# Optimization experiments

Measured on AMD Instinct MI355X. Metric: run time of the kernel, lower is better.

The kernel has to match this reference:

```python
import jax, jax.numpy as jnp
import numpy as np

D_MODEL = 1024
H = 16
D_K = D_MODEL // H
B, S = 4, 2048
NEG = -1000000000.0


def setup_inputs() -> dict:
    key = jax.random.key(0)
    ks = jax.random.split(key, 12)
    scale = 1.0 / np.sqrt(D_MODEL)
    inp = {
        "query": jax.random.normal(ks[0], (B, S, D_MODEL), jnp.float32),
        "key": jax.random.normal(ks[1], (B, S, D_MODEL), jnp.float32),
        "value": jax.random.normal(ks[2], (B, S, D_MODEL), jnp.float32),
        # causal lower-triangular mask, shape (B, S, S); forward unsqueezes head dim
        "mask": jnp.broadcast_to(jnp.tril(jnp.ones((S, S), jnp.int32)), (B, S, S)),
        "Wq": jax.random.normal(ks[3], (D_MODEL, D_MODEL), jnp.float32) * scale,
        "bq": jnp.zeros((D_MODEL,), jnp.float32),
        "Wk": jax.random.normal(ks[4], (D_MODEL, D_MODEL), jnp.float32) * scale,
        "bk": jnp.zeros((D_MODEL,), jnp.float32),
        "Wv": jax.random.normal(ks[5], (D_MODEL, D_MODEL), jnp.float32) * scale,
        "bv": jnp.zeros((D_MODEL,), jnp.float32),
        "Wo": jax.random.normal(ks[6], (D_MODEL, D_MODEL), jnp.float32) * scale,
        "bo": jnp.zeros((D_MODEL,), jnp.float32),
    }
    return inp


def reference(query, key, value, mask, Wq, bq, Wk, bk, Wv, bv, Wo, bo):
    b, s, _ = query.shape
    # projections (torch Linear: x @ W.T + b); split into heads -> (b, h, s, d_k)
    def proj(x, W, bias):
        return (x @ W.T + bias).reshape(b, -1, H, D_K).transpose(0, 2, 1, 3)

    Q = proj(query, Wq, bq)
    K = proj(key, Wk, bk)
    V = proj(value, Wv, bv)

    scores = jnp.einsum("bhqd,bhkd->bhqk", Q, K) / np.sqrt(D_K)
    m = mask[:, None, :, :]  # (b, 1, s, s)
    scores = jnp.where(m == 0, NEG, scores)
    attn = jax.nn.softmax(scores, axis=-1)
    x = jnp.einsum("bhqk,bhkd->bhqd", attn, V)
    x = x.transpose(0, 2, 1, 3).reshape(b, -1, D_MODEL)
    return x @ Wo.T + bo
```

## Files before the change

kernel.cpp:

```cpp
#include <hip/hip_runtime.h>
#include <hip/hip_bf16.h>

#define DMODEL 1024
#define NH 16
#define DKH 64
#define NB 4
#define SEQ 2048
#define MTOT (NB*SEQ)

typedef __bf16 bf16_t;
typedef __bf16 bf16x8 __attribute__((ext_vector_type(8)));
typedef float f32x4 __attribute__((ext_vector_type(4)));

__device__ __forceinline__ void async_copy16(void* lds, const void* g) {
    __builtin_amdgcn_global_load_lds(
        (const __attribute__((address_space(1))) unsigned int*)g,
        (__attribute__((address_space(3))) unsigned int*)lds, 16, 0, 0);
}

__device__ __forceinline__ float fast_exp2(float x) {
    return __builtin_amdgcn_exp2f(x);
}

__device__ __forceinline__ float rsum16(float v) {
    v += __shfl_xor(v, 1);
    v += __shfl_xor(v, 2);
    v += __shfl_xor(v, 4);
    v += __shfl_xor(v, 8);
    return v;
}

__global__ void cvt_kernel(const float* __restrict__ s0, const float* __restrict__ s1,
                           const float* __restrict__ s2, const float* __restrict__ s3,
                           bf16_t* __restrict__ d0, bf16_t* __restrict__ d1,
                           bf16_t* __restrict__ d2, bf16_t* __restrict__ d3, int n)
{
    const float* s = (blockIdx.y == 0) ? s0 : (blockIdx.y == 1) ? s1 :
                     (blockIdx.y == 2) ? s2 : s3;
    bf16_t* d = (blockIdx.y == 0) ? d0 : (blockIdx.y == 1) ? d1 :
                (blockIdx.y == 2) ? d2 : d3;
    int i = (blockIdx.x * 256 + threadIdx.x) * 8;
    if (i < n) {
        float4 a = *(const float4*)&s[i];
        float4 b = *(const float4*)&s[i + 4];
        union { bf16_t h[8]; uint4 u; } t;
        t.h[0]=(bf16_t)a.x; t.h[1]=(bf16_t)a.y; t.h[2]=(bf16_t)a.z; t.h[3]=(bf16_t)a.w;
        t.h[4]=(bf16_t)b.x; t.h[5]=(bf16_t)b.y; t.h[6]=(bf16_t)b.z; t.h[7]=(bf16_t)b.w;
        *(uint4*)&d[i] = t.u;
    }
}

template<int OUT_MODE>
__global__ __launch_bounds__(256, 3)
void gemm_bt(const bf16_t* __restrict__ A, const bf16_t* __restrict__ W,
             const float* __restrict__ bias, void* __restrict__ out,
             int M, int N, int K, float scale)
{
    __shared__ bf16_t As[128 * 64];
    __shared__ bf16_t Ws[128 * 64];

    const int tid  = threadIdx.x;
    const int wave = tid >> 6;
    const int lane = tid & 63;
    const int ln   = lane & 15;
    const int quad = lane >> 4;
    const int wm   = (wave >> 1) * 64;
    const int wn   = (wave & 1) * 64;
    const int bm   = blockIdx.x * 128;
    const int bn   = blockIdx.y * 128;
    const int srow = wave * 8 + (lane >> 3);
    const int sg   = (lane & 7) * 8;

    f32x4 acc[4][4] = {};

    for (int k0 = 0; k0 < K; k0 += 64) {
        #pragma unroll
        for (int rr = 0; rr < 4; ++rr) {
            int row = rr * 32 + srow;
            async_copy16(&As[(size_t)(rr * 32 + wave * 8) * 64],
                         &A[(size_t)(bm + row) * K + k0 + sg]);
            async_copy16(&Ws[(size_t)(rr * 32 + wave * 8) * 64],
                         &W[(size_t)(bn + row) * K + k0 + sg]);
        }
        __syncthreads();

        bf16x8 af[2][4], wf[2][4];
        #pragma unroll
        for (int h = 0; h < 2; ++h)
            #pragma unroll
            for (int u = 0; u < 4; ++u) {
                af[h][u] = *(const bf16x8*)&As[(wm + u * 16 + ln) * 64 + h * 32 + quad * 8];
                wf[h][u] = *(const bf16x8*)&Ws[(wn + u * 16 + ln) * 64 + h * 32 + quad * 8];
            }
        #pragma unroll
        for (int h = 0; h < 2; ++h)
            #pragma unroll
            for (int im = 0; im < 4; ++im)
                #pragma unroll
                for (int jn = 0; jn < 4; ++jn)
                    acc[im][jn] = __builtin_amdgcn_mfma_f32_16x16x32_bf16(
                        af[h][im], wf[h][jn], acc[im][jn], 0, 0, 0);

        __syncthreads();
    }

    #pragma unroll
    for (int jn = 0; jn < 4; ++jn) {
        int n = bn + wn + jn * 16 + ln;
        float bv = bias[n];
        #pragma unroll
        for (int im = 0; im < 4; ++im) {
            #pragma unroll
            for (int r = 0; r < 4; ++r) {
                int m = bm + wm + im * 16 + quad * 4 + r;
                float v = (acc[im][jn][r] + bv) * scale;
                if (OUT_MODE == 0) {
                    int b = m >> 11, s = m & (SEQ - 1);
                    int h = n >> 6, d = n & 63;
                    ((bf16_t*)out)[(((size_t)(b * NH + h)) * SEQ + s) * DKH + d] = (bf16_t)v;
                } else if (OUT_MODE == 2) {
                    int b = m >> 11, s = m & (SEQ - 1);
                    int h = n >> 6, d = n & 63;
                    ((bf16_t*)out)[(((size_t)(b * NH + h)) * DKH + d) * SEQ + s] = (bf16_t)v;
                } else {
                    ((float*)out)[(size_t)m * N + n] = v;
                }
            }
        }
    }
}

__global__ __launch_bounds__(256, 3)
void gemm_qkv(const bf16_t* __restrict__ Aq, const bf16_t* __restrict__ Ak,
              const bf16_t* __restrict__ Av, const bf16_t* __restrict__ W3,
              const float* __restrict__ bqp, const float* __restrict__ bkp,
              const float* __restrict__ bvp,
              bf16_t* __restrict__ Qh, bf16_t* __restrict__ Kh,
              bf16_t* __restrict__ Vth, float qscale)
{
    __shared__ bf16_t As[128 * 64];
    __shared__ bf16_t Ws[128 * 64];

    const int K    = DMODEL;
    const int tid  = threadIdx.x;
    const int wave = tid >> 6;
    const int lane = tid & 63;
    const int ln   = lane & 15;
    const int quad = lane >> 4;
    const int wm   = (wave >> 1) * 64;
    const int wn   = (wave & 1) * 64;
    const int bm   = blockIdx.x * 128;
    const int bnG  = blockIdx.y * 128;
    const int sel  = blockIdx.y >> 3;
    const bf16_t* A = (sel == 0) ? Aq : (sel == 1) ? Ak : Av;
    const int srow = wave * 8 + (lane >> 3);
    const int sg   = (lane & 7) * 8;

    f32x4 acc[4][4] = {};

    for (int k0 = 0; k0 < K; k0 += 64) {
        #pragma unroll
        for (int rr = 0; rr < 4; ++rr) {
            int row = rr * 32 + srow;
            async_copy16(&As[(size_t)(rr * 32 + wave * 8) * 64],
                         &A[(size_t)(bm + row) * K + k0 + sg]);
            async_copy16(&Ws[(size_t)(rr * 32 + wave * 8) * 64],
                         &W3[(size_t)(bnG + row) * K + k0 + sg]);
        }
        __syncthreads();

        bf16x8 af[2][4], wf[2][4];
        #pragma unroll
        for (int h = 0; h < 2; ++h)
            #pragma unroll
            for (int u = 0; u < 4; ++u) {
                af[h][u] = *(const bf16x8*)&As[(wm + u * 16 + ln) * 64 + h * 32 + quad * 8];
                wf[h][u] = *(const bf16x8*)&Ws[(wn + u * 16 + ln) * 64 + h * 32 + quad * 8];
            }
        #pragma unroll
        for (int h = 0; h < 2; ++h)
            #pragma unroll
            for (int im = 0; im < 4; ++im)
                #pragma unroll
                for (int jn = 0; jn < 4; ++jn)
                    acc[im][jn] = __builtin_amdgcn_mfma_f32_16x16x32_bf16(
                        af[h][im], wf[h][jn], acc[im][jn], 0, 0, 0);

        __syncthreads();
    }

    const float* bias = (sel == 0) ? bqp : (sel == 1) ? bkp : bvp;
    const float scale = (sel == 0) ? qscale : 1.0f;
    const int bn = bnG & (DMODEL - 1);

    #pragma unroll
    for (int jn = 0; jn < 4; ++jn) {
        int n = bn + wn + jn * 16 + ln;
        float bv = bias[n];
        int h = n >> 6, d = n & 63;
        #pragma unroll
        for (int im = 0; im < 4; ++im) {
            #pragma unroll
            for (int r = 0; r < 4; ++r) {
                int m = bm + wm + im * 16 + quad * 4 + r;
                float v = (acc[im][jn][r] + bv) * scale;
                int b = m >> 11, s = m & (SEQ - 1);
                if (sel == 2) {
                    Vth[(((size_t)(b * NH + h)) * DKH + d) * SEQ + s] = (bf16_t)v;
                } else {
                    bf16_t* outp = (sel == 1) ? Kh : Qh;
                    outp[(((size_t)(b * NH + h)) * SEQ + s) * DKH + d] = (bf16_t)v;
                }
            }
        }
    }
}

__global__ __launch_bounds__(256, 3)
void attn_kernel(const bf16_t* __restrict__ Q, const bf16_t* __restrict__ Km,
                 const bf16_t* __restrict__ Vt, bf16_t* __restrict__ X)
{
    __shared__ __align__(16) bf16_t Ks[2][64 * 64];
    __shared__ __align__(16) bf16_t Vs[2][64 * 64];
    __shared__ __align__(16) bf16_t Ps[4][32][72];

    const int tid  = threadIdx.x;
    const int wave = tid >> 6;
    const int lane = tid & 63;
    const int ln   = lane & 15;
    const int quad = lane >> 4;
    const int cs   = ln & 7;

    const int qt = (blockIdx.x + blockIdx.y + ((blockIdx.y >> 4) << 2)) & 15;
    const int bh = blockIdx.y;
    const int q0 = qt * 128;
    const size_t base = (size_t)bh * SEQ * DKH;

    bf16x8 aq[2][2];
    #pragma unroll
    for (int so = 0; so < 2; ++so) {
        const bf16_t* qr = Q + base + (size_t)(q0 + so * 64 + wave * 16 + ln) * DKH;
        aq[so][0] = *(const bf16x8*)(qr + quad * 8);
        aq[so][1] = *(const bf16x8*)(qr + 32 + quad * 8);
    }

    f32x4 oacc[2][4] = {};
    float psum[2][4] = {};

    const int nkt = 2 * qt + 2;

    const int srow8 = lane >> 3;
    const int schk  = lane & 7;

    #pragma unroll
    for (int qq = 0; qq < 2; ++qq) {
        const int rb  = wave * 16 + qq * 8;
        const int row = rb + srow8;
        const int csr = schk ^ (row & 7);
        async_copy16(&Ks[0][rb * 64], Km + base + (size_t)row * DKH + csr * 8);
        async_copy16(&Vs[0][rb * 64], Vt + base + (size_t)row * SEQ + csr * 8);
    }
    __syncthreads();

    int cur = 0;
    for (int kt = 0; kt < nkt; ++kt, cur ^= 1) {
        const int j0 = kt * 64;
        const bool skip0 = (kt == nkt - 1);

        if (kt + 1 < nkt) {
            const int jn0 = j0 + 64;
            #pragma unroll
            for (int qq = 0; qq < 2; ++qq) {
                const int rb  = wave * 16 + qq * 8;
                const int row = rb + srow8;
                const int csr = schk ^ (row & 7);
                async_copy16(&Ks[cur ^ 1][rb * 64],
                             Km + base + (size_t)(jn0 + row) * DKH + csr * 8);
                async_copy16(&Vs[cur ^ 1][rb * 64],
                             Vt + base + (size_t)row * SEQ + jn0 + csr * 8);
            }
        }

        bf16x8 kf[4][2];
        #pragma unroll
        for (int jn = 0; jn < 4; ++jn) {
            const int rr = (jn * 16 + ln) * 64;
            kf[jn][0] = *(const bf16x8*)&Ks[cur][rr + ((quad    ) ^ cs) * 8];
            kf[jn][1] = *(const bf16x8*)&Ks[cur][rr + ((4 + quad) ^ cs) * 8];
        }

        f32x4 s[2][4] = {};
        #pragma unroll
        for (int so = 0; so < 2; ++so) {
            if (so == 0 && skip0) continue;
            #pragma unroll
            for (int jn = 0; jn < 4; ++jn) {
                s[so][jn] = __builtin_amdgcn_mfma_f32_16x16x32_bf16(aq[so][0], kf[jn][0], s[so][jn], 0, 0, 0);
                s[so][jn] = __builtin_amdgcn_mfma_f32_16x16x32_bf16(aq[so][1], kf[jn][1], s[so][jn], 0, 0, 0);
            }
        }

        bf16x8 vf[4][2];
        #pragma unroll
        for (int nj = 0; nj < 4; ++nj) {
            const int rr = (nj * 16 + ln) * 64;
            vf[nj][0] = *(const bf16x8*)&Vs[cur][rr + ((quad    ) ^ cs) * 8];
            vf[nj][1] = *(const bf16x8*)&Vs[cur][rr + ((4 + quad) ^ cs) * 8];
        }

        #pragma unroll
        for (int so = 0; so < 2; ++so) {
            if (so == 0 && skip0) continue;
            const int rbase = q0 + so * 64 + wave * 16 + quad * 4;
            const bool diag = (j0 + 63 > q0 + so * 64);
            #pragma unroll
            for (int r = 0; r < 4; ++r) {
                float rowsum = 0.f;
                #pragma unroll
                for (int jn = 0; jn < 4; ++jn) {
                    float v = s[so][jn][r];
                    if (diag) {
                        int col = j0 + jn * 16 + ln;
                        if (col > rbase + r) v = -1e30f;
                    }
                    float p = fast_exp2(v);
                    s[so][jn][r] = p;
                    rowsum += p;
                }
                psum[so][r] += rowsum;
            }
            #pragma unroll
            for (int r = 0; r < 4; ++r)
                #pragma unroll
                for (int jn = 0; jn < 4; ++jn)
                    Ps[wave][so * 16 + quad * 4 + r][jn * 16 + ln] = (bf16_t)s[so][jn][r];
        }

        #pragma unroll
        for (int so = 0; so < 2; ++so) {
            if (so == 0 && skip0) continue;
            bf16x8 ap0 = *(const bf16x8*)&Ps[wave][so * 16 + ln][quad * 8];
            bf16x8 ap1 = *(const bf16x8*)&Ps[wave][so * 16 + ln][32 + quad * 8];
            #pragma unroll
            for (int nj = 0; nj < 4; ++nj) {
                oacc[so][nj] = __builtin_amdgcn_mfma_f32_16x16x32_bf16(ap0, vf[nj][0], oacc[so][nj], 0, 0, 0);
                oacc[so][nj] = __builtin_amdgcn_mfma_f32_16x16x32_bf16(ap1, vf[nj][1], oacc[so][nj], 0, 0, 0);
            }
        }

        __syncthreads();
    }

    const int bb = bh >> 4, hh = bh & 15;
    #pragma unroll
    for (int so = 0; so < 2; ++so) {
        #pragma unroll
        for (int r = 0; r < 4; ++r) {
            int sg = q0 + so * 64 + wave * 16 + quad * 4 + r;
            float inv = 1.f / rsum16(psum[so][r]);
            #pragma unroll
            for (int nj = 0; nj < 4; ++nj)
                X[((size_t)(bb * SEQ + sg)) * DMODEL + hh * DKH + nj * 16 + ln] =
                    (bf16_t)(oacc[so][nj][r] * inv);
        }
    }
}

extern "C" void kernel_launch(void* const* d_in, const int* in_sizes, int n_in,
                              void* d_out, int out_size, void* d_ws, size_t ws_size,
                              hipStream_t stream)
{
    const float* query = (const float*)d_in[0];
    const float* key   = (const float*)d_in[1];
    const float* value = (const float*)d_in[2];
    const float* Wq = (const float*)d_in[4];
    const float* bq = (const float*)d_in[5];
    const float* Wk = (const float*)d_in[6];
    const float* bk = (const float*)d_in[7];
    const float* Wv = (const float*)d_in[8];
    const float* bv = (const float*)d_in[9];
    const float* Wo = (const float*)d_in[10];
    const float* bo = (const float*)d_in[11];
    float* out = (float*)d_out;

    char* ws = (char*)d_ws;
    bf16_t* qb  = (bf16_t*)(ws);
    bf16_t* kb  = (bf16_t*)(ws + ((size_t)16 << 20));
    bf16_t* vb  = (bf16_t*)(ws + ((size_t)32 << 20));
    bf16_t* Qh  = (bf16_t*)(ws + ((size_t)48 << 20));
    bf16_t* Wqb = (bf16_t*)(ws + ((size_t)64 << 20));
    bf16_t* Wkb = (bf16_t*)(ws + ((size_t)66 << 20));
    bf16_t* Wvb = (bf16_t*)(ws + ((size_t)68 << 20));
    bf16_t* Wob = (bf16_t*)(ws + ((size_t)70 << 20));
    bf16_t* Kh  = (bf16_t*)d_out;
    bf16_t* Vth = (bf16_t*)((char*)d_out + ((size_t)16 << 20));
    bf16_t* X   = qb;

    const int nAct = MTOT * DMODEL;
    const int nW   = DMODEL * DMODEL;
    cvt_kernel<<<dim3(nAct / 2048, 3), 256, 0, stream>>>(query, key, value, query,
                                                         qb, kb, vb, qb, nAct);
    cvt_kernel<<<dim3(nW / 2048, 4), 256, 0, stream>>>(Wq, Wk, Wv, Wo,
                                                       Wqb, Wkb, Wvb, Wob, nW);

    dim3 bt(256);
    const float qscale = 0.125f * 1.4426950408889634f;

    gemm_qkv<<<dim3(MTOT / 128, 3 * DMODEL / 128), bt, 0, stream>>>(
        qb, kb, vb, Wqb, bq, bk, bv, Qh, Kh, Vth, qscale);

    attn_kernel<<<dim3(SEQ / 128, NB * NH), bt, 0, stream>>>(Qh, Kh, Vth, X);

    gemm_bt<1><<<dim3(MTOT / 128, DMODEL / 128), bt, 0, stream>>>(
        X, Wob, bo, out, MTOT, DMODEL, DMODEL, 1.0f);
}
```

Baseline: 393.6 us.

## Fuse fp32-to-bf16 activation conversion into QKV GEMM and swizzle LDS tiles

Removes the separate activation conversion kernel. The QKV GEMM now loads fp32 inputs through registers with a one-tile-ahead prefetch, converts them to bf16 and writes them to LDS with an XOR swizzle to avoid bank conflicts. The attention kernel shrinks its P staging buffer to one 16-row swizzled tile per wave and raises launch bounds occupancy to 4. This saves a full write and read of the bf16 activations, but the GEMM now reads the fp32 A tile (twice the bytes) eight times, once per N-tile, and adds register pressure from the prefetch.

```diff
diff --git a/kernel.cpp b/kernel.cpp
--- a/kernel.cpp
+++ b/kernel.cpp
@@ -114,34 +114,23 @@
             for (int r = 0; r < 4; ++r) {
                 int m = bm + wm + im * 16 + quad * 4 + r;
                 float v = (acc[im][jn][r] + bv) * scale;
-                if (OUT_MODE == 0) {
-                    int b = m >> 11, s = m & (SEQ - 1);
-                    int h = n >> 6, d = n & 63;
-                    ((bf16_t*)out)[(((size_t)(b * NH + h)) * SEQ + s) * DKH + d] = (bf16_t)v;
-                } else if (OUT_MODE == 2) {
-                    int b = m >> 11, s = m & (SEQ - 1);
-                    int h = n >> 6, d = n & 63;
-                    ((bf16_t*)out)[(((size_t)(b * NH + h)) * DKH + d) * SEQ + s] = (bf16_t)v;
-                } else {
-                    ((float*)out)[(size_t)m * N + n] = v;
-                }
+                ((float*)out)[(size_t)m * N + n] = v;
             }
         }
     }
 }
 
 __global__ __launch_bounds__(256, 3)
-void gemm_qkv(const bf16_t* __restrict__ Aq, const bf16_t* __restrict__ Ak,
-              const bf16_t* __restrict__ Av, const bf16_t* __restrict__ W3,
+void gemm_qkv(const float* __restrict__ Aq32, const float* __restrict__ Ak32,
+              const float* __restrict__ Av32, const bf16_t* __restrict__ W3,
               const float* __restrict__ bqp, const float* __restrict__ bkp,
               const float* __restrict__ bvp,
               bf16_t* __restrict__ Qh, bf16_t* __restrict__ Kh,
               bf16_t* __restrict__ Vth, float qscale)
 {
-    __shared__ bf16_t As[128 * 64];
-    __shared__ bf16_t Ws[128 * 64];
-
-    const int K    = DMODEL;
+    __shared__ __align__(16) bf16_t As[128 * 64];
+    __shared__ __align__(16) bf16_t Ws[128 * 64];
+
     const int tid  = threadIdx.x;
     const int wave = tid >> 6;
     const int lane = tid & 63;
@@ -152,40 +141,75 @@
     const int bm   = blockIdx.x * 128;
     const int bnG  = blockIdx.y * 128;
     const int sel  = blockIdx.y >> 3;
-    const bf16_t* A = (sel == 0) ? Aq : (sel == 1) ? Ak : Av;
+    const float* A32 = (sel == 0) ? Aq32 : (sel == 1) ? Ak32 : Av32;
     const int srow = wave * 8 + (lane >> 3);
     const int sg   = (lane & 7) * 8;
 
+    const int ar = tid >> 2;
+    const int ac = (tid & 3) * 16;
+    const int acb = ac >> 3;
+
     f32x4 acc[4][4] = {};
-
-    for (int k0 = 0; k0 < K; k0 += 64) {
+    float4 pf[2][4];
+
+    #pragma unroll
+    for (int h2 = 0; h2 < 2; ++h2) {
+        const float* p = A32 + (size_t)(bm + h2 * 64 + ar) * DMODEL + ac;
+        pf[h2][0] = *(const float4*)(p);
+        pf[h2][1] = *(const float4*)(p + 4);
+        pf[h2][2] = *(const float4*)(p + 8);
+        pf[h2][3] = *(const float4*)(p + 12);
+    }
+
+    for (int k0 = 0; k0 < DMODEL; k0 += 64) {
         #pragma unroll
         for (int rr = 0; rr < 4; ++rr) {
             int row = rr * 32 + srow;
-            async_copy16(&As[(size_t)(rr * 32 + wave * 8) * 64],
-                         &A[(size_t)(bm + row) * K + k0 + sg]);
             async_copy16(&Ws[(size_t)(rr * 32 + wave * 8) * 64],
-                         &W3[(size_t)(bnG + row) * K + k0 + sg]);
+                         &W3[(size_t)(bnG + row) * DMODEL + k0 + sg]);
+        }
+        #pragma unroll
+        for (int h2 = 0; h2 < 2; ++h2) {
+            const int row = h2 * 64 + ar;
+            const int sw  = row & 7;
+            union { bf16_t h[16]; uint4 u[2]; } t;
+            #pragma unroll
+            for (int j = 0; j < 4; ++j) {
+                float4 v = pf[h2][j];
+                t.h[j*4+0] = (bf16_t)v.x; t.h[j*4+1] = (bf16_t)v.y;
+                t.h[j*4+2] = (bf16_t)v.z; t.h[j*4+3] = (bf16_t)v.w;
+            }
+            *(uint4*)&As[row * 64 + ((acb ^ sw) << 3)]       = t.u[0];
+            *(uint4*)&As[row * 64 + (((acb + 1) ^ sw) << 3)] = t.u[1];
+        }
+        if (k0 + 64 < DMODEL) {
+            #pragma unroll
+            for (int h2 = 0; h2 < 2; ++h2) {
+                const float* p = A32 + (size_t)(bm + h2 * 64 + ar) * DMODEL + k0 + 64 + ac;
+                pf[h2][0] = *(const float4*)(p);
+                pf[h2][1] = *(const float4*)(p + 4);
+                pf[h2][2] = *(const float4*)(p + 8);
+                pf[h2][3] = *(const float4*)(p + 12);
+            }
         }
         __syncthreads();
 
-        bf16x8 af[2][4], wf[2][4];
-        #pragma unroll
-        for (int h = 0; h < 2; ++h)
+        #pragma unroll
+        for (int h = 0; h < 2; ++h) {
+            bf16x8 af[4], wf[4];
             #pragma unroll
             for (int u = 0; u < 4; ++u) {
-                af[h][u] = *(const bf16x8*)&As[(wm + u * 16 + ln) * 64 + h * 32 + quad * 8];
-                wf[h][u] = *(const bf16x8*)&Ws[(wn + u * 16 + ln) * 64 + h * 32 + quad * 8];
-            }
-        #pragma unroll
-        for (int h = 0; h < 2; ++h)
+                af[u] = *(const bf16x8*)&As[(wm + u * 16 + ln) * 64 +
+                                            (((h * 4 + quad) ^ (ln & 7)) << 3)];
+                wf[u] = *(const bf16x8*)&Ws[(wn + u * 16 + ln) * 64 + h * 32 + quad * 8];
+            }
             #pragma unroll
             for (int im = 0; im < 4; ++im)
                 #pragma unroll
                 for (int jn = 0; jn < 4; ++jn)
                     acc[im][jn] = __builtin_amdgcn_mfma_f32_16x16x32_bf16(
-                        af[h][im], wf[h][jn], acc[im][jn], 0, 0, 0);
-
+                        af[im], wf[jn], acc[im][jn], 0, 0, 0);
+        }
         __syncthreads();
     }
 
@@ -216,13 +240,13 @@
     }
 }
 
-__global__ __launch_bounds__(256, 3)
+__global__ __launch_bounds__(256, 4)
 void attn_kernel(const bf16_t* __restrict__ Q, const bf16_t* __restrict__ Km,
                  const bf16_t* __restrict__ Vt, bf16_t* __restrict__ X)
 {
     __shared__ __align__(16) bf16_t Ks[2][64 * 64];
     __shared__ __align__(16) bf16_t Vs[2][64 * 64];
-    __shared__ __align__(16) bf16_t Ps[4][32][72];
+    __shared__ __align__(16) bf16_t Ps[4][16][64];
 
     const int tid  = threadIdx.x;
     const int wave = tid >> 6;
@@ -330,17 +354,15 @@
                 psum[so][r] += rowsum;
             }
             #pragma unroll
-            for (int r = 0; r < 4; ++r)
+            for (int r = 0; r < 4; ++r) {
+                const int row = quad * 4 + r, sw = row & 7;
                 #pragma unroll
                 for (int jn = 0; jn < 4; ++jn)
-                    Ps[wave][so * 16 + quad * 4 + r][jn * 16 + ln] = (bf16_t)s[so][jn][r];
-        }
-
-        #pragma unroll
-        for (int so = 0; so < 2; ++so) {
-            if (so == 0 && skip0) continue;
-            bf16x8 ap0 = *(const bf16x8*)&Ps[wave][so * 16 + ln][quad * 8];
-            bf16x8 ap1 = *(const bf16x8*)&Ps[wave][so * 16 + ln][32 + quad * 8];
+                    Ps[wave][row][(((jn * 2 + (ln >> 3)) ^ sw) << 3) + (ln & 7)] =
+                        (bf16_t)s[so][jn][r];
+            }
+            bf16x8 ap0 = *(const bf16x8*)&Ps[wave][ln][((quad       ^ (ln & 7)) << 3)];
+            bf16x8 ap1 = *(const bf16x8*)&Ps[wave][ln][(((4 + quad) ^ (ln & 7)) << 3)];
             #pragma unroll
             for (int nj = 0; nj < 4; ++nj) {
                 oacc[so][nj] = __builtin_amdgcn_mfma_f32_16x16x32_bf16(ap0, vf[nj][0], oacc[so][nj], 0, 0, 0);
@@ -384,9 +406,7 @@
     float* out = (float*)d_out;
 
     char* ws = (char*)d_ws;
-    bf16_t* qb  = (bf16_t*)(ws);
-    bf16_t* kb  = (bf16_t*)(ws + ((size_t)16 << 20));
-    bf16_t* vb  = (bf16_t*)(ws + ((size_t)32 << 20));
+    bf16_t* X   = (bf16_t*)(ws);
     bf16_t* Qh  = (bf16_t*)(ws + ((size_t)48 << 20));
     bf16_t* Wqb = (bf16_t*)(ws + ((size_t)64 << 20));
     bf16_t* Wkb = (bf16_t*)(ws + ((size_t)66 << 20));
@@ -394,12 +414,8 @@
     bf16_t* Wob = (bf16_t*)(ws + ((size_t)70 << 20));
     bf16_t* Kh  = (bf16_t*)d_out;
     bf16_t* Vth = (bf16_t*)((char*)d_out + ((size_t)16 << 20));
-    bf16_t* X   = qb;
-
-    const int nAct = MTOT * DMODEL;
-    const int nW   = DMODEL * DMODEL;
-    cvt_kernel<<<dim3(nAct / 2048, 3), 256, 0, stream>>>(query, key, value, query,
-                                                         qb, kb, vb, qb, nAct);
+
+    const int nW = DMODEL * DMODEL;
     cvt_kernel<<<dim3(nW / 2048, 4), 256, 0, stream>>>(Wq, Wk, Wv, Wo,
                                                        Wqb, Wkb, Wvb, Wob, nW);
 
@@ -407,7 +423,7 @@
     const float qscale = 0.125f * 1.4426950408889634f;
 
     gemm_qkv<<<dim3(MTOT / 128, 3 * DMODEL / 128), bt, 0, stream>>>(
-        qb, kb, vb, Wqb, bq, bk, bv, Qh, Kh, Vth, qscale);
+        query, key, value, Wqb, bq, bk, bv, Qh, Kh, Vth, qscale);
 
     attn_kernel<<<dim3(SEQ / 128, NB * NH), bt, 0, stream>>>(Qh, Kh, Vth, X);
 
```

Result: slower. 471.4 us (+19.7%).

## Pair complementary causal query tiles per attention block for load balance

Applied to the files above, without the earlier changes.

Each attention block now handles two query tiles, qt and 15-qt, so every block does a similar amount of causal work. K/V tiles loaded once serve both query tiles, which halves the block count and shares K/V loads. Launch bounds drop to 2 blocks per CU to make room for the doubled accumulator and Q registers. The unused OUT_MODE branches of the generic GEMM epilogue are also removed.

```diff
diff --git a/kernel.cpp b/kernel.cpp
--- a/kernel.cpp
+++ b/kernel.cpp
@@ -114,17 +114,7 @@
             for (int r = 0; r < 4; ++r) {
                 int m = bm + wm + im * 16 + quad * 4 + r;
                 float v = (acc[im][jn][r] + bv) * scale;
-                if (OUT_MODE == 0) {
-                    int b = m >> 11, s = m & (SEQ - 1);
-                    int h = n >> 6, d = n & 63;
-                    ((bf16_t*)out)[(((size_t)(b * NH + h)) * SEQ + s) * DKH + d] = (bf16_t)v;
-                } else if (OUT_MODE == 2) {
-                    int b = m >> 11, s = m & (SEQ - 1);
-                    int h = n >> 6, d = n & 63;
-                    ((bf16_t*)out)[(((size_t)(b * NH + h)) * DKH + d) * SEQ + s] = (bf16_t)v;
-                } else {
-                    ((float*)out)[(size_t)m * N + n] = v;
-                }
+                ((float*)out)[(size_t)m * N + n] = v;
             }
         }
     }
@@ -216,7 +206,7 @@
     }
 }
 
-__global__ __launch_bounds__(256, 3)
+__global__ __launch_bounds__(256, 2)
 void attn_kernel(const bf16_t* __restrict__ Q, const bf16_t* __restrict__ Km,
                  const bf16_t* __restrict__ Vt, bf16_t* __restrict__ X)
 {
@@ -231,23 +221,26 @@
     const int quad = lane >> 4;
     const int cs   = ln & 7;
 
-    const int qt = (blockIdx.x + blockIdx.y + ((blockIdx.y >> 4) << 2)) & 15;
-    const int bh = blockIdx.y;
-    const int q0 = qt * 128;
+    const int bh  = blockIdx.x;
+    const int qtA = blockIdx.y;
+    const int qtB = 15 - qtA;
+    const int q0A = qtA * 128;
+    const int q0B = qtB * 128;
     const size_t base = (size_t)bh * SEQ * DKH;
 
-    bf16x8 aq[2][2];
+    bf16x8 aq[4][2];
     #pragma unroll
-    for (int so = 0; so < 2; ++so) {
-        const bf16_t* qr = Q + base + (size_t)(q0 + so * 64 + wave * 16 + ln) * DKH;
-        aq[so][0] = *(const bf16x8*)(qr + quad * 8);
-        aq[so][1] = *(const bf16x8*)(qr + 32 + quad * 8);
-    }
-
-    f32x4 oacc[2][4] = {};
-    float psum[2][4] = {};
-
-    const int nkt = 2 * qt + 2;
+    for (int st = 0; st < 4; ++st) {
+        const int sb = ((st < 2) ? q0A : q0B) + (st & 1) * 64;
+        const bf16_t* qr = Q + base + (size_t)(sb + wave * 16 + ln) * DKH;
+        aq[st][0] = *(const bf16x8*)(qr + quad * 8);
+        aq[st][1] = *(const bf16x8*)(qr + 32 + quad * 8);
+    }
+
+    f32x4 oacc[4][4] = {};
+    float psum[4][4] = {};
+
+    const int nkt = 2 * qtB + 2;
 
     const int srow8 = lane >> 3;
     const int schk  = lane & 7;
@@ -265,7 +258,6 @@
     int cur = 0;
     for (int kt = 0; kt < nkt; ++kt, cur ^= 1) {
         const int j0 = kt * 64;
-        const bool skip0 = (kt == nkt - 1);
 
         if (kt + 1 < nkt) {
             const int jn0 = j0 + 64;
@@ -288,18 +280,6 @@
             kf[jn][0] = *(const bf16x8*)&Ks[cur][rr + ((quad    ) ^ cs) * 8];
             kf[jn][1] = *(const bf16x8*)&Ks[cur][rr + ((4 + quad) ^ cs) * 8];
         }
-
-        f32x4 s[2][4] = {};
-        #pragma unroll
-        for (int so = 0; so < 2; ++so) {
-            if (so == 0 && skip0) continue;
-            #pragma unroll
-            for (int jn = 0; jn < 4; ++jn) {
-                s[so][jn] = __builtin_amdgcn_mfma_f32_16x16x32_bf16(aq[so][0], kf[jn][0], s[so][jn], 0, 0, 0);
-                s[so][jn] = __builtin_amdgcn_mfma_f32_16x16x32_bf16(aq[so][1], kf[jn][1], s[so][jn], 0, 0, 0);
-            }
-        }
-
         bf16x8 vf[4][2];
         #pragma unroll
         for (int nj = 0; nj < 4; ++nj) {
@@ -309,42 +289,58 @@
         }
 
         #pragma unroll
-        for (int so = 0; so < 2; ++so) {
-            if (so == 0 && skip0) continue;
-            const int rbase = q0 + so * 64 + wave * 16 + quad * 4;
-            const bool diag = (j0 + 63 > q0 + so * 64);
-            #pragma unroll
-            for (int r = 0; r < 4; ++r) {
-                float rowsum = 0.f;
+        for (int pair = 0; pair < 2; ++pair) {
+            const int q0p = (pair == 0) ? q0A : q0B;
+
+            f32x4 s[2][4] = {};
+            #pragma unroll
+            for (int sl = 0; sl < 2; ++sl) {
+                const int st = pair * 2 + sl;
+                const int sb = q0p + sl * 64;
+                if (j0 > sb + 63) continue;
                 #pragma unroll
                 for (int jn = 0; jn < 4; ++jn) {
-                    float v = s[so][jn][r];
-                    if (diag) {
-                        int col = j0 + jn * 16 + ln;
-                        if (col > rbase + r) v = -1e30f;
+                    s[sl][jn] = __builtin_amdgcn_mfma_f32_16x16x32_bf16(aq[st][0], kf[jn][0], s[sl][jn], 0, 0, 0);
+                    s[sl][jn] = __builtin_amdgcn_mfma_f32_16x16x32_bf16(aq[st][1], kf[jn][1], s[sl][jn], 0, 0, 0);
+                }
+            }
+
+            #pragma unroll
+            for (int sl = 0; sl < 2; ++sl) {
+                const int st = pair * 2 + sl;
+                const int sb = q0p + sl * 64;
+                if (j0 > sb + 63) continue;
+                const int rbase = sb + wave * 16 + quad * 4;
+                const bool diag = (j0 + 63 > sb);
+                #pragma unroll
+                for (int r = 0; r < 4; ++r) {
+                    float rowsum = 0.f;
+                    #pragma unroll
+                    for (int jn = 0; jn < 4; ++jn) {
+                        float v = s[sl][jn][r];
+                        if (diag) {
+                            int col = j0 + jn * 16 + ln;
+                            if (col > rbase + r) v = -1e30f;
+                        }
+                        float p = fast_exp2(v);
+                        s[sl][jn][r] = p;
+                        rowsum += p;
                     }
-                    float p = fast_exp2(v);
-                    s[so][jn][r] = p;
-                    rowsum += p;
+                    psum[st][r] += rowsum;
                 }
-                psum[so][r] += rowsum;
-            }
-            #pragma unroll
-            for (int r = 0; r < 4; ++r)
-                #pragma unroll
-                for (int jn = 0; jn < 4; ++jn)
-                    Ps[wave][so * 16 + quad * 4 + r][jn * 16 + ln] = (bf16_t)s[so][jn][r];
-        }
-
-        #pragma unroll
-        for (int so = 0; so < 2; ++so) {
-            if (so == 0 && skip0) continue;
-            bf16x8 ap0 = *(const bf16x8*)&Ps[wave][so * 16 + ln][quad * 8];
-            bf16x8 ap1 = *(const bf16x8*)&Ps[wave][so * 16 + ln][32 + quad * 8];
-            #pragma unroll
-            for (int nj = 0; nj < 4; ++nj) {
-                oacc[so][nj] = __builtin_amdgcn_mfma_f32_16x16x32_bf16(ap0, vf[nj][0], oacc[so][nj], 0, 0, 0);
-                oacc[so][nj] = __builtin_amdgcn_mfma_f32_16x16x32_bf16(ap1, vf[nj][1], oacc[so][nj], 0, 0, 0);
+                #pragma unroll
+                for (int r = 0; r < 4; ++r)
+                    #pragma unroll
+                    for (int jn = 0; jn < 4; ++jn)
+                        Ps[wave][sl * 16 + quad * 4 + r][jn * 16 + ln] = (bf16_t)s[sl][jn][r];
+
+                bf16x8 ap0 = *(const bf16x8*)&Ps[wave][sl * 16 + ln][quad * 8];
+                bf16x8 ap1 = *(const bf16x8*)&Ps[wave][sl * 16 + ln][32 + quad * 8];
+                #pragma unroll
+                for (int nj = 0; nj < 4; ++nj) {
+                    oacc[st][nj] = __builtin_amdgcn_mfma_f32_16x16x32_bf16(ap0, vf[nj][0], oacc[st][nj], 0, 0, 0);
+                    oacc[st][nj] = __builtin_amdgcn_mfma_f32_16x16x32_bf16(ap1, vf[nj][1], oacc[st][nj], 0, 0, 0);
+                }
             }
         }
 
@@ -353,15 +349,16 @@
 
     const int bb = bh >> 4, hh = bh & 15;
     #pragma unroll
-    for (int so = 0; so < 2; ++so) {
+    for (int st = 0; st < 4; ++st) {
+        const int sb = ((st < 2) ? q0A : q0B) + (st & 1) * 64;
         #pragma unroll
         for (int r = 0; r < 4; ++r) {
-            int sg = q0 + so * 64 + wave * 16 + quad * 4 + r;
-            float inv = 1.f / rsum16(psum[so][r]);
+            int sg = sb + wave * 16 + quad * 4 + r;
+            float inv = 1.f / rsum16(psum[st][r]);
             #pragma unroll
             for (int nj = 0; nj < 4; ++nj)
                 X[((size_t)(bb * SEQ + sg)) * DMODEL + hh * DKH + nj * 16 + ln] =
-                    (bf16_t)(oacc[so][nj][r] * inv);
+                    (bf16_t)(oacc[st][nj][r] * inv);
         }
     }
 }
@@ -409,7 +406,7 @@
     gemm_qkv<<<dim3(MTOT / 128, 3 * DMODEL / 128), bt, 0, stream>>>(
         qb, kb, vb, Wqb, bq, bk, bv, Qh, Kh, Vth, qscale);
 
-    attn_kernel<<<dim3(SEQ / 128, NB * NH), bt, 0, stream>>>(Qh, Kh, Vth, X);
+    attn_kernel<<<dim3(NB * NH, SEQ / 256), bt, 0, stream>>>(Qh, Kh, Vth, X);
 
     gemm_bt<1><<<dim3(MTOT / 128, DMODEL / 128), bt, 0, stream>>>(
         X, Wob, bo, out, MTOT, DMODEL, DMODEL, 1.0f);
```

Result: faster. 374.3 us (-4.9%).
